# Optimization experiments

Hardware: AMD Instinct MI355X
Metric: run time of the kernel (lower is better)

The kernel has to match this reference:

```python
import jax, jax.numpy as jnp
import numpy as np
import math

B, H, S, D = 8, 16, 1024, 64


def setup_inputs() -> dict:
    key = jax.random.key(0)
    kq, kk, kv, kl = jax.random.split(key, 4)
    queries = jax.random.normal(kq, (B * H, S, D), dtype=jnp.float32)
    keys = jax.random.normal(kk, (B * H, S, D), dtype=jnp.float32)
    values = jax.random.normal(kv, (B * H, S, D), dtype=jnp.float32)
    valid_lens = jax.random.randint(kl, (B,), 0, 1024, dtype=jnp.int64)
    return {"queries": queries, "keys": keys, "values": values, "valid_lens": valid_lens}


def reference(queries, keys, values, valid_lens):
    d = queries.shape[-1]
    seq_len = queries.shape[1]
    b = valid_lens.shape[0]
    h = queries.shape[0] // b
    scale = 1.0 / math.sqrt(d)
    # [BH, S, S] scores, faithful to bmm(q, k^T)/sqrt(d)
    scores = jnp.einsum("bqd,bkd->bqk", queries, keys) * scale
    # encode_mask: mask[b, q, k] = (k >= valid_lens[b]) for 1-D valid_lens
    key_mask = jnp.arange(seq_len) >= valid_lens[:, None]  # [B, S]
    scores = scores.reshape(b, h, seq_len, seq_len)
    # masked_fill with 1e-6 (NOT -inf), faithful to the original
    scores = jnp.where(key_mask[:, None, None, :], jnp.float32(1e-6), scores)
    attn = jax.nn.softmax(scores, axis=-1)
    out = jnp.einsum("bhqk,bhkd->bhqd", attn, values.reshape(b, h, seq_len, d))
    return out.reshape(b * h, seq_len, d)
```

## Files before the change

kernel.cpp:

```cpp
#include <hip/hip_runtime.h>
#include <hip/hip_bf16.h>

typedef short short4v __attribute__((ext_vector_type(4)));
typedef short short8v __attribute__((ext_vector_type(8)));
typedef float floatx4 __attribute__((ext_vector_type(4)));
typedef unsigned int uint2v __attribute__((ext_vector_type(2)));

#define SLEN 1024
#define DDIM 64
#define NBH  128

__device__ __forceinline__ unsigned short f2bf(float f) {
  union { float f; unsigned int u; } v; v.f = f;
  unsigned int u = v.u;
  u += 0x7fffu + ((u >> 16) & 1u);
  return (unsigned short)(u >> 16);
}

__device__ __forceinline__ unsigned int pkbf(float a, float b) {
  __hip_bfloat162 h = __float22bfloat162_rn(float2{a, b});
  union { __hip_bfloat162 h; unsigned int u; } c; c.h = h;
  return c.u;
}

__device__ __forceinline__ void pl32sw(unsigned int &a, unsigned int &b) {
#if __has_builtin(__builtin_amdgcn_permlane32_swap)
  uint2v r = __builtin_amdgcn_permlane32_swap(a, b, false, false);
  a = r[0]; b = r[1];
#else
  asm volatile("s_nop 1\n\tv_permlane32_swap_b32 %0, %1" : "+v"(a), "+v"(b));
#endif
}
__device__ __forceinline__ void pl16sw(unsigned int &a, unsigned int &b) {
#if __has_builtin(__builtin_amdgcn_permlane16_swap)
  uint2v r = __builtin_amdgcn_permlane16_swap(a, b, false, false);
  a = r[0]; b = r[1];
#else
  asm volatile("s_nop 1\n\tv_permlane16_swap_b32 %0, %1" : "+v"(a), "+v"(b));
#endif
}

__device__ __forceinline__ int decode_vl(const int* __restrict__ vraw, int bh) {
  const bool is64 = (vraw[1] == 0) && (vraw[3] == 0) && (vraw[5] == 0) && (vraw[7] == 0);
  const int b = bh >> 4;
  return is64 ? vraw[2 * b] : vraw[b];
}
__device__ __forceinline__ int nch_of(const int* __restrict__ vraw, int bh) {
  const int v = decode_vl(vraw, bh);
  return (v >> 6) + ((v & 63) ? 1 : 0);
}

__global__ __launch_bounds__(256)
void prep(const float* __restrict__ Vg, const int* __restrict__ vraw,
          float* __restrict__ SV2, int* __restrict__ TL) {
  if (blockIdx.x < NBH) {
    const int bh = blockIdx.x;
    const int d  = threadIdx.x & 63;
    const int cg = threadIdx.x >> 6;
    const int ts = nch_of(vraw, bh);
    float sum = 0.f;
    for (int ch = ts + cg; ch < 16; ch += 4) {
      const float* src = Vg + (size_t)(bh * SLEN + ch * 64) * DDIM + d;
      #pragma unroll
      for (int k = 0; k < 64; ++k) sum += src[(size_t)k * DDIM];
    }
    __shared__ float red[4][64];
    red[cg][d] = sum;
    __syncthreads();
    if (cg == 0)
      SV2[(size_t)bh * 64 + d] = (red[0][d] + red[1][d]) + (red[2][d] + red[3][d]);
  } else {
    __shared__ int gs[NBH];
    const int x = threadIdx.x;
    if (x < NBH) {
      const int ni = nch_of(vraw, x);
      int rank = 0;
      for (int j = 0; j < NBH; ++j) {
        const int nj = nch_of(vraw, j);
        rank += (int)((nj > ni) || (nj == ni && j < x));
      }
      gs[rank] = x;
    }
    __syncthreads();
    if (x < NBH) {
      const int bh = gs[x];
      #pragma unroll
      for (int qb = 0; qb < 8; ++qb) TL[x * 8 + qb] = bh | (qb << 8);
    }
  }
}

__global__ __launch_bounds__(256)
void attn_main(const float* __restrict__ Qg, const float* __restrict__ Kg,
               const float* __restrict__ Vg, const float* __restrict__ SV,
               const int* __restrict__ TL, const int* __restrict__ vraw,
               float* __restrict__ Og)
{
  __shared__ unsigned short K_lds[2][4096];
  __shared__ unsigned short VT_lds[2][4096];

  const int t  = threadIdx.x;
  const int ww = t >> 6;
  const int ln = t & 15;
  const int g  = (t >> 4) & 3;

  int bh, q0;
  if (TL) {
    const int te = TL[blockIdx.x];
    bh = te & 127;
    q0 = ((te >> 8) & 7) * 128;
  } else {
    bh = blockIdx.x & 127;
    q0 = (blockIdx.x >> 7) * 128;
  }

  const int vl          = decode_vl(vraw, bh);
  const int full_ch     = vl >> 6;
  const int has_partial = (vl & 63) ? 1 : 0;
  const int nch         = SV ? (full_ch + has_partial) : 16;
  const int tail_start  = full_ch + has_partial;

  const float qs = 0.125f * 1.44269504f;
  short8v bq[2][2];
  #pragma unroll
  for (int nt = 0; nt < 2; ++nt) {
    const float* qp = Qg + ((size_t)bh * SLEN + q0 + ww * 32 + nt * 16 + ln) * DDIM;
    #pragma unroll
    for (int st = 0; st < 2; ++st) {
      const float4 f0 = *(const float4*)(qp + st * 32 + g * 8);
      const float4 f1 = *(const float4*)(qp + st * 32 + g * 8 + 4);
      short8v a;
      a[0]=(short)f2bf(f0.x*qs); a[1]=(short)f2bf(f0.y*qs);
      a[2]=(short)f2bf(f0.z*qs); a[3]=(short)f2bf(f0.w*qs);
      a[4]=(short)f2bf(f1.x*qs); a[5]=(short)f2bf(f1.y*qs);
      a[6]=(short)f2bf(f1.z*qs); a[7]=(short)f2bf(f1.w*qs);
      bq[nt][st] = a;
    }
  }

  const int l7  = ln & 7;
  const int sw0 = ((g) ^ l7) * 8;
  const int sw1 = ((4 + g) ^ l7) * 8;

  short8v ones;
  #pragma unroll
  for (int j = 0; j < 8; ++j) ones[j] = (short)0x3F80;

  floatx4 ot[2][4], lacc[2];
  #pragma unroll
  for (int m = 0; m < 2; ++m) {
    lacc[m] = (floatx4){0.f, 0.f, 0.f, 0.f};
    #pragma unroll
    for (int f = 0; f < 4; ++f) ot[m][f] = (floatx4){0.f, 0.f, 0.f, 0.f};
  }

  float kr[2][8];
  float vlo[8], vhi[8];
  const int dv = t & 31;
  const int gv = t >> 5;
  const float* kbB = Kg + (size_t)bh * SLEN * DDIM;
  const float* vbB = Vg + (size_t)bh * SLEN * DDIM;

  auto stage_load = [&](int ch) {
    const float* kb_ = kbB + (size_t)ch * 64 * DDIM;
    const float* vb_ = vbB + (size_t)ch * 64 * DDIM;
    #pragma unroll
    for (int h = 0; h < 2; ++h) {
      const int q = t + h * 256;
      const int r = q >> 3, gr = q & 7;
      const float4 f0 = *(const float4*)(kb_ + r * DDIM + gr * 8);
      const float4 f1 = *(const float4*)(kb_ + r * DDIM + gr * 8 + 4);
      kr[h][0]=f0.x; kr[h][1]=f0.y; kr[h][2]=f0.z; kr[h][3]=f0.w;
      kr[h][4]=f1.x; kr[h][5]=f1.y; kr[h][6]=f1.z; kr[h][7]=f1.w;
    }
    #pragma unroll
    for (int j = 0; j < 8; ++j) {
      vlo[j] = vb_[(gv * 8 + j) * DDIM + dv];
      vhi[j] = vb_[(gv * 8 + j) * DDIM + dv + 32];
    }
  };
  auto stage_write = [&](int b) {
    #pragma unroll
    for (int h = 0; h < 2; ++h) {
      const int q = t + h * 256;
      const int r = q >> 3, gr = q & 7;
      union { short8v s; unsigned int u[4]; } ks;
      ks.u[0] = pkbf(kr[h][0], kr[h][1]);
      ks.u[1] = pkbf(kr[h][2], kr[h][3]);
      ks.u[2] = pkbf(kr[h][4], kr[h][5]);
      ks.u[3] = pkbf(kr[h][6], kr[h][7]);
      *(short8v*)&K_lds[b][r * 64 + ((gr ^ (r & 7)) * 8)] = ks.s;
    }
    union { short8v s; unsigned int u[4]; } va, vb2;
    va.u[0]  = pkbf(vlo[0], vlo[1]); va.u[1]  = pkbf(vlo[2], vlo[3]);
    va.u[2]  = pkbf(vlo[4], vlo[5]); va.u[3]  = pkbf(vlo[6], vlo[7]);
    vb2.u[0] = pkbf(vhi[0], vhi[1]); vb2.u[1] = pkbf(vhi[2], vhi[3]);
    vb2.u[2] = pkbf(vhi[4], vhi[5]); vb2.u[3] = pkbf(vhi[6], vhi[7]);
    const int swv = (gv ^ (dv & 7)) * 8;
    *(short8v*)&VT_lds[b][dv * 64 + swv] = va.s;
    *(short8v*)&VT_lds[b][(dv + 32) * 64 + swv] = vb2.s;
  };

  if (nch > 0) {
    stage_load(0);
    stage_write(0);
    if (nch > 1) stage_load(1);
    asm volatile("s_waitcnt lgkmcnt(0)" ::: "memory");
    __builtin_amdgcn_s_barrier();
    asm volatile("" ::: "memory");
  }

  for (int ch = 0; ch < nch; ++ch) {
    const int b = ch & 1;
    if (ch + 1 < nch) stage_write(b ^ 1);
    if (ch + 2 < nch) stage_load(ch + 2);

    floatx4 c[4][2];
    __builtin_amdgcn_s_setprio(1);
    #pragma unroll
    for (int mt = 0; mt < 4; ++mt) {
      const short8v a0 = *(const short8v*)&K_lds[b][(mt * 16 + ln) * 64 + sw0];
      const short8v a1 = *(const short8v*)&K_lds[b][(mt * 16 + ln) * 64 + sw1];
      #pragma unroll
      for (int nt = 0; nt < 2; ++nt) {
        floatx4 acc = (floatx4){0.f, 0.f, 0.f, 0.f};
        acc = __builtin_amdgcn_mfma_f32_16x16x32_bf16(a0, bq[nt][0], acc, 0, 0, 0);
        acc = __builtin_amdgcn_mfma_f32_16x16x32_bf16(a1, bq[nt][1], acc, 0, 0, 0);
        c[mt][nt] = acc;
      }
    }
    __builtin_amdgcn_s_setprio(0);

    unsigned int pk0[4][2], pk1[4][2];
    const bool fullv = (ch < full_ch);
    #pragma unroll
    for (int mt = 0; mt < 4; ++mt) {
      const int kg = ch * 64 + mt * 16 + g * 4;
      #pragma unroll
      for (int nt = 0; nt < 2; ++nt) {
        float p[4];
        if (fullv) {
          #pragma unroll
          for (int i = 0; i < 4; ++i) p[i] = __builtin_amdgcn_exp2f(c[mt][nt][i]);
        } else {
          #pragma unroll
          for (int i = 0; i < 4; ++i) {
            const float x = (kg + i < vl) ? c[mt][nt][i] : 0.0f;
            p[i] = __builtin_amdgcn_exp2f(x);
          }
        }
        pk0[mt][nt] = pkbf(p[0], p[1]);
        pk1[mt][nt] = pkbf(p[2], p[3]);
      }
    }

    short8v bp[2][2];
    #pragma unroll
    for (int st = 0; st < 2; ++st) {
      #pragma unroll
      for (int nt = 0; nt < 2; ++nt) {
        unsigned int a0 = pk0[2 * st][nt], b0 = pk0[2 * st + 1][nt];
        unsigned int a1 = pk1[2 * st][nt], b1 = pk1[2 * st + 1][nt];
        pl32sw(a0, b0); pl16sw(a0, b0);
        pl32sw(a1, b1); pl16sw(a1, b1);
        union { short8v s; unsigned int u[4]; } bb;
        bb.u[0] = a0; bb.u[1] = a1; bb.u[2] = b0; bb.u[3] = b1;
        bp[st][nt] = bb.s;
      }
    }

    __builtin_amdgcn_s_setprio(1);
    #pragma unroll
    for (int st = 0; st < 2; ++st) {
      lacc[0] = __builtin_amdgcn_mfma_f32_16x16x32_bf16(ones, bp[st][0], lacc[0], 0, 0, 0);
      lacc[1] = __builtin_amdgcn_mfma_f32_16x16x32_bf16(ones, bp[st][1], lacc[1], 0, 0, 0);
      const int sw = (st == 0) ? sw0 : sw1;
      #pragma unroll
      for (int f = 0; f < 4; ++f) {
        const short8v av = *(const short8v*)&VT_lds[b][(f * 16 + ln) * 64 + sw];
        ot[0][f] = __builtin_amdgcn_mfma_f32_16x16x32_bf16(av, bp[st][0], ot[0][f], 0, 0, 0);
        ot[1][f] = __builtin_amdgcn_mfma_f32_16x16x32_bf16(av, bp[st][1], ot[1][f], 0, 0, 0);
      }
    }
    __builtin_amdgcn_s_setprio(0);

    if (ch + 1 < nch) {
      asm volatile("s_waitcnt lgkmcnt(0)" ::: "memory");
      __builtin_amdgcn_s_barrier();
      asm volatile("" ::: "memory");
    }
  }

  if (SV != nullptr && tail_start < 16) {
    const float* sv = SV + (size_t)bh * 64 + g * 4;
    float4 sv4[4];
    #pragma unroll
    for (int f = 0; f < 4; ++f) sv4[f] = *(const float4*)(sv + f * 16);
    const float ml = (float)(SLEN - tail_start * 64);
    #pragma unroll
    for (int nt = 0; nt < 2; ++nt) {
      #pragma unroll
      for (int i = 0; i < 4; ++i) lacc[nt][i] += ml;
      #pragma unroll
      for (int f = 0; f < 4; ++f) {
        ot[nt][f][0] += sv4[f].x; ot[nt][f][1] += sv4[f].y;
        ot[nt][f][2] += sv4[f].z; ot[nt][f][3] += sv4[f].w;
      }
    }
  }

  #pragma unroll
  for (int nt = 0; nt < 2; ++nt) {
    const float inv = 1.0f / lacc[nt][0];
    float* orow = Og + ((size_t)bh * SLEN + q0 + ww * 32 + nt * 16 + ln) * DDIM + g * 4;
    #pragma unroll
    for (int f = 0; f < 4; ++f) {
      float4 v4;
      v4.x = ot[nt][f][0] * inv; v4.y = ot[nt][f][1] * inv;
      v4.z = ot[nt][f][2] * inv; v4.w = ot[nt][f][3] * inv;
      *(float4*)(orow + f * 16) = v4;
    }
  }
}

extern "C" void kernel_launch(void* const* d_in, const int* in_sizes, int n_in,
                              void* d_out, int out_size, void* d_ws, size_t ws_size,
                              hipStream_t stream) {
  const float* Q = (const float*)d_in[0];
  const float* K = (const float*)d_in[1];
  const float* V = (const float*)d_in[2];
  const int*  vl = (const int*)d_in[3];
  float* out = (float*)d_out;

  const size_t off_tl = (size_t)NBH * 64 * 4;
  const size_t ws_all = off_tl + 1024 * 4;

  if (ws_size >= ws_all) {
    float* SV2 = (float*)d_ws;
    int*   TL  = (int*)((char*)d_ws + off_tl);
    prep<<<NBH + 1, 256, 0, stream>>>(V, vl, SV2, TL);
    attn_main<<<dim3(1024), dim3(256), 0, stream>>>(Q, K, V, SV2, TL, vl, out);
  } else {
    attn_main<<<dim3(1024), dim3(256), 0, stream>>>(Q, K, V, nullptr, nullptr, vl, out);
  }
}
```

Measured before the change: 165.3 us.

## Deepen K/V register prefetch to two buffers, drop work sorting and setprio

The main loop now keeps two register staging sets for K/V, so global loads are issued three chunks ahead instead of two, giving memory latency more time to hide behind MFMA work. The prep kernel no longer sorts (batch, head) pairs by chunk count to build a longest-first tile list, and attention blocks fall back to a direct blockIdx mapping. The s_setprio hints around the MFMA sections are also removed. The extra staging registers raise register pressure, and with valid lengths varying per batch, dropping the sorted order can leave load imbalance at the tail of the grid.

```diff
diff --git a/kernel.cpp b/kernel.cpp
--- a/kernel.cpp
+++ b/kernel.cpp
@@ -52,49 +52,28 @@
 
 __global__ __launch_bounds__(256)
 void prep(const float* __restrict__ Vg, const int* __restrict__ vraw,
-          float* __restrict__ SV2, int* __restrict__ TL) {
-  if (blockIdx.x < NBH) {
-    const int bh = blockIdx.x;
-    const int d  = threadIdx.x & 63;
-    const int cg = threadIdx.x >> 6;
-    const int ts = nch_of(vraw, bh);
-    float sum = 0.f;
-    for (int ch = ts + cg; ch < 16; ch += 4) {
-      const float* src = Vg + (size_t)(bh * SLEN + ch * 64) * DDIM + d;
-      #pragma unroll
-      for (int k = 0; k < 64; ++k) sum += src[(size_t)k * DDIM];
-    }
-    __shared__ float red[4][64];
-    red[cg][d] = sum;
-    __syncthreads();
-    if (cg == 0)
-      SV2[(size_t)bh * 64 + d] = (red[0][d] + red[1][d]) + (red[2][d] + red[3][d]);
-  } else {
-    __shared__ int gs[NBH];
-    const int x = threadIdx.x;
-    if (x < NBH) {
-      const int ni = nch_of(vraw, x);
-      int rank = 0;
-      for (int j = 0; j < NBH; ++j) {
-        const int nj = nch_of(vraw, j);
-        rank += (int)((nj > ni) || (nj == ni && j < x));
-      }
-      gs[rank] = x;
-    }
-    __syncthreads();
-    if (x < NBH) {
-      const int bh = gs[x];
-      #pragma unroll
-      for (int qb = 0; qb < 8; ++qb) TL[x * 8 + qb] = bh | (qb << 8);
-    }
-  }
+          float* __restrict__ SV2) {
+  const int bh = blockIdx.x;
+  const int d  = threadIdx.x & 63;
+  const int cg = threadIdx.x >> 6;
+  const int ts = nch_of(vraw, bh);
+  float sum = 0.f;
+  for (int ch = ts + cg; ch < 16; ch += 4) {
+    const float* src = Vg + (size_t)(bh * SLEN + ch * 64) * DDIM + d;
+    #pragma unroll
+    for (int k = 0; k < 64; ++k) sum += src[(size_t)k * DDIM];
+  }
+  __shared__ float red[4][64];
+  red[cg][d] = sum;
+  __syncthreads();
+  if (cg == 0)
+    SV2[(size_t)bh * 64 + d] = (red[0][d] + red[1][d]) + (red[2][d] + red[3][d]);
 }
 
 __global__ __launch_bounds__(256)
 void attn_main(const float* __restrict__ Qg, const float* __restrict__ Kg,
                const float* __restrict__ Vg, const float* __restrict__ SV,
-               const int* __restrict__ TL, const int* __restrict__ vraw,
-               float* __restrict__ Og)
+               const int* __restrict__ vraw, float* __restrict__ Og)
 {
   __shared__ unsigned short K_lds[2][4096];
   __shared__ unsigned short VT_lds[2][4096];
@@ -104,15 +83,8 @@
   const int ln = t & 15;
   const int g  = (t >> 4) & 3;
 
-  int bh, q0;
-  if (TL) {
-    const int te = TL[blockIdx.x];
-    bh = te & 127;
-    q0 = ((te >> 8) & 7) * 128;
-  } else {
-    bh = blockIdx.x & 127;
-    q0 = (blockIdx.x >> 7) * 128;
-  }
+  const int bh = blockIdx.x & 127;
+  const int q0 = (blockIdx.x >> 7) * 128;
 
   const int vl          = decode_vl(vraw, bh);
   const int full_ch     = vl >> 6;
@@ -154,14 +126,14 @@
     for (int f = 0; f < 4; ++f) ot[m][f] = (floatx4){0.f, 0.f, 0.f, 0.f};
   }
 
-  float kr[2][8];
-  float vlo[8], vhi[8];
+  float kra[2][8], krb[2][8];
+  float vloa[8], vhia[8], vlob[8], vhib[8];
   const int dv = t & 31;
   const int gv = t >> 5;
   const float* kbB = Kg + (size_t)bh * SLEN * DDIM;
   const float* vbB = Vg + (size_t)bh * SLEN * DDIM;
 
-  auto stage_load = [&](int ch) {
+  auto stage_load = [&](int ch, float (&kr)[2][8], float (&vlo)[8], float (&vhi)[8]) {
     const float* kb_ = kbB + (size_t)ch * 64 * DDIM;
     const float* vb_ = vbB + (size_t)ch * 64 * DDIM;
     #pragma unroll
@@ -179,7 +151,7 @@
       vhi[j] = vb_[(gv * 8 + j) * DDIM + dv + 32];
     }
   };
-  auto stage_write = [&](int b) {
+  auto stage_write = [&](int b, float (&kr)[2][8], float (&vlo)[8], float (&vhi)[8]) {
     #pragma unroll
     for (int h = 0; h < 2; ++h) {
       const int q = t + h * 256;
@@ -201,22 +173,13 @@
     *(short8v*)&VT_lds[b][(dv + 32) * 64 + swv] = vb2.s;
   };
 
-  if (nch > 0) {
-    stage_load(0);
-    stage_write(0);
-    if (nch > 1) stage_load(1);
-    asm volatile("s_waitcnt lgkmcnt(0)" ::: "memory");
-    __builtin_amdgcn_s_barrier();
-    asm volatile("" ::: "memory");
-  }
-
-  for (int ch = 0; ch < nch; ++ch) {
-    const int b = ch & 1;
-    if (ch + 1 < nch) stage_write(b ^ 1);
-    if (ch + 2 < nch) stage_load(ch + 2);
+  auto iter = [&](int ch, int b,
+                  float (&wkr)[2][8], float (&wvlo)[8], float (&wvhi)[8],
+                  float (&lkr)[2][8], float (&lvlo)[8], float (&lvhi)[8]) {
+    if (ch + 1 < nch) stage_write(b ^ 1, wkr, wvlo, wvhi);
+    if (ch + 3 < nch) stage_load(ch + 3, lkr, lvlo, lvhi);
 
     floatx4 c[4][2];
-    __builtin_amdgcn_s_setprio(1);
     #pragma unroll
     for (int mt = 0; mt < 4; ++mt) {
       const short8v a0 = *(const short8v*)&K_lds[b][(mt * 16 + ln) * 64 + sw0];
@@ -229,7 +192,6 @@
         c[mt][nt] = acc;
       }
     }
-    __builtin_amdgcn_s_setprio(0);
 
     unsigned int pk0[4][2], pk1[4][2];
     const bool fullv = (ch < full_ch);
@@ -269,7 +231,6 @@
       }
     }
 
-    __builtin_amdgcn_s_setprio(1);
     #pragma unroll
     for (int st = 0; st < 2; ++st) {
       lacc[0] = __builtin_amdgcn_mfma_f32_16x16x32_bf16(ones, bp[st][0], lacc[0], 0, 0, 0);
@@ -282,12 +243,32 @@
         ot[1][f] = __builtin_amdgcn_mfma_f32_16x16x32_bf16(av, bp[st][1], ot[1][f], 0, 0, 0);
       }
     }
-    __builtin_amdgcn_s_setprio(0);
 
     if (ch + 1 < nch) {
       asm volatile("s_waitcnt lgkmcnt(0)" ::: "memory");
       __builtin_amdgcn_s_barrier();
       asm volatile("" ::: "memory");
+    }
+  };
+
+  if (nch > 0) {
+    stage_load(0, kra, vloa, vhia);
+    stage_write(0, kra, vloa, vhia);
+    if (nch > 1) stage_load(1, krb, vlob, vhib);
+    if (nch > 2) stage_load(2, kra, vloa, vhia);
+    asm volatile("s_waitcnt lgkmcnt(0)" ::: "memory");
+    __builtin_amdgcn_s_barrier();
+    asm volatile("" ::: "memory");
+  }
+
+  {
+    int ch = 0;
+    while (ch < nch) {
+      iter(ch, 0, krb, vlob, vhib, krb, vlob, vhib);
+      ++ch;
+      if (ch >= nch) break;
+      iter(ch, 1, kra, vloa, vhia, kra, vloa, vhia);
+      ++ch;
     }
   }
 
@@ -332,15 +313,13 @@
   const int*  vl = (const int*)d_in[3];
   float* out = (float*)d_out;
 
-  const size_t off_tl = (size_t)NBH * 64 * 4;
-  const size_t ws_all = off_tl + 1024 * 4;
+  const size_t ws_all = (size_t)NBH * 64 * 4;
 
   if (ws_size >= ws_all) {
     float* SV2 = (float*)d_ws;
-    int*   TL  = (int*)((char*)d_ws + off_tl);
-    prep<<<NBH + 1, 256, 0, stream>>>(V, vl, SV2, TL);
-    attn_main<<<dim3(1024), dim3(256), 0, stream>>>(Q, K, V, SV2, TL, vl, out);
+    prep<<<NBH, 256, 0, stream>>>(V, vl, SV2);
+    attn_main<<<dim3(1024), dim3(256), 0, stream>>>(Q, K, V, SV2, vl, out);
   } else {
-    attn_main<<<dim3(1024), dim3(256), 0, stream>>>(Q, K, V, nullptr, nullptr, vl, out);
-  }
-}
+    attn_main<<<dim3(1024), dim3(256), 0, stream>>>(Q, K, V, nullptr, vl, out);
+  }
+}
```

Result: slower. 186.9 us (+13.1%).
